# Kernel tuning notes

Hardware: AMD Instinct MI355X
Metric: run time of the kernel (lower is better)

## Reference

```python
import jax, jax.numpy as jnp
import numpy as np

B, C_IN, C_TMP, C_OUT, N = 4, 256, 256, 256, 4096


def setup_inputs() -> dict:
    key = jax.random.key(0)
    k1, k2, k3, k4 = jax.random.split(key, 4)
    scale = 1.0 / np.sqrt(C_IN)
    return {
        "fea": jax.random.normal(k1, (B, C_IN, N), dtype=jnp.float32),
        "Wq": jax.random.normal(k2, (C_TMP, C_IN), dtype=jnp.float32) * scale,
        "Wk": jax.random.normal(k3, (C_TMP, C_IN), dtype=jnp.float32) * scale,
        "Wv": jax.random.normal(k4, (C_OUT, C_IN), dtype=jnp.float32) * scale,
    }


def reference(fea, Wq, Wk, Wv):
    # 1x1 Conv1d == per-point channel matmul
    Q = jnp.einsum("ti,bin->btn", Wq, fea)   # (B, temp, N)
    K = jnp.einsum("ti,bin->btn", Wk, fea)   # (B, temp, N)
    V = jnp.einsum("oi,bin->bon", Wv, fea)   # (B, out, N)
    # S[b, i, j] = sum_t K[b, t, i] * Q[b, t, j]; note: no 1/sqrt(d) scaling
    S = jnp.einsum("bti,btj->bij", K, Q)     # (B, N, N)
    S = jax.nn.softmax(S, axis=1)            # softmax over key axis (dim=1)
    new_fea = jnp.einsum("bok,bkn->bon", V, S)  # (B, out, N)
    # merge == 'concat'
    out = jnp.concatenate([new_fea, fea], axis=1)  # (B, out+in, N)
    return jax.nn.relu(out)
```

## Files before the change

### kernel.cpp

```cpp
#include <hip/hip_runtime.h>

#define NB 4
#define C  256
#define NN 4096

typedef _Float16 half8   __attribute__((ext_vector_type(8)));
typedef _Float16 h2      __attribute__((ext_vector_type(2)));
typedef float    f32x4   __attribute__((ext_vector_type(4)));
typedef float    f32x16  __attribute__((ext_vector_type(16)));

static __device__ __forceinline__ f32x4 mfma16(half8 a, half8 b, f32x4 c) {
    return __builtin_amdgcn_mfma_f32_16x16x32_f16(a, b, c, 0, 0, 0);
}
static __device__ __forceinline__ f32x16 mfma32(half8 a, half8 b, f32x16 c) {
    return __builtin_amdgcn_mfma_f32_32x32x16_f16(a, b, c, 0, 0, 0);
}
static __device__ __forceinline__ void gld16(const void* g, void* l) {
    __builtin_amdgcn_global_load_lds(
        (const __attribute__((address_space(1))) unsigned int*)g,
        (__attribute__((address_space(3))) unsigned int*)l, 16, 0, 0);
}
static __device__ __forceinline__ h2 cvtpk(float a, float b) {
    auto r = __builtin_amdgcn_cvt_pkrtz(a, b);
    return *reinterpret_cast<h2*>(&r);
}
static __device__ __forceinline__ unsigned cvtpk_u(float a, float b) {
    auto r = __builtin_amdgcn_cvt_pkrtz(a, b);
    return *reinterpret_cast<unsigned*>(&r);
}

__global__ __launch_bounds__(256) void proj_kernel(
    const float* __restrict__ fea, const float* __restrict__ Wq,
    const float* __restrict__ Wk, const float* __restrict__ Wv,
    _Float16* __restrict__ Qt, _Float16* __restrict__ Kt,
    _Float16* __restrict__ Vp, float* __restrict__ out)
{
    const int lin = blockIdx.x + gridDim.x * blockIdx.y;
    const int xcd = lin & 7;
    const int b   = xcd >> 1;
    const int nt  = ((lin >> 3) << 1) | (xcd & 1);
    const int n0  = nt * 32;

    __shared__ __align__(16) _Float16 fh[32][264];

    const int tid = threadIdx.x;
    {
        const int nl = tid & 31, rr = tid >> 5;
        const float* feab = fea + (size_t)b * C * NN + n0 + nl;
        float* outb = out + (size_t)b * 2 * C * NN + (size_t)C * NN + n0 + nl;
#pragma unroll
        for (int p = 0; p < 32; ++p) {
            const int i = p * 8 + rr;
            const float v = feab[(size_t)i * NN];
            outb[(size_t)i * NN] = fmaxf(v, 0.f);
            fh[nl][i] = (_Float16)v;
        }
    }
    __syncthreads();

    const int w = tid >> 6, lane = tid & 63, lr = lane & 15, lg = lane >> 4;

    const float* const Ws[2] = {Wq, Wk};
    _Float16* const   Od[2] = {Qt + (size_t)b * NN * C, Kt + (size_t)b * NN * C};
#pragma unroll 1
    for (int qk = 0; qk < 2; ++qk) {
        const float* __restrict__ W = Ws[qk];
        f32x4 acc[2][4];
#pragma unroll
        for (int mi = 0; mi < 2; ++mi)
#pragma unroll
            for (int ni = 0; ni < 4; ++ni) acc[mi][ni] = (f32x4){0.f, 0.f, 0.f, 0.f};

#pragma unroll 1
        for (int kt = 0; kt < 8; ++kt) {
            half8 ah[2];
#pragma unroll
            for (int mi = 0; mi < 2; ++mi)
                ah[mi] = *(const half8*)&fh[mi * 16 + lr][kt * 32 + lg * 8];
            half8 bh[4];
#pragma unroll
            for (int ni = 0; ni < 4; ++ni) {
                const float* src = W + (size_t)(w * 64 + ni * 16 + lr) * C + kt * 32 + lg * 8;
                const float4 x0 = *(const float4*)src;
                const float4 x1 = *(const float4*)(src + 4);
                bh[ni][0] = (_Float16)x0.x; bh[ni][1] = (_Float16)x0.y;
                bh[ni][2] = (_Float16)x0.z; bh[ni][3] = (_Float16)x0.w;
                bh[ni][4] = (_Float16)x1.x; bh[ni][5] = (_Float16)x1.y;
                bh[ni][6] = (_Float16)x1.z; bh[ni][7] = (_Float16)x1.w;
            }
#pragma unroll
            for (int mi = 0; mi < 2; ++mi)
#pragma unroll
                for (int ni = 0; ni < 4; ++ni)
                    acc[mi][ni] = mfma16(ah[mi], bh[ni], acc[mi][ni]);
        }
        _Float16* dst = Od[qk];
#pragma unroll
        for (int mi = 0; mi < 2; ++mi)
#pragma unroll
            for (int ni = 0; ni < 4; ++ni)
#pragma unroll
                for (int r = 0; r < 4; ++r)
                    dst[(size_t)(n0 + mi * 16 + lg * 4 + r) * C + (w * 64 + ni * 16 + lr)] =
                        (_Float16)acc[mi][ni][r];
    }

    {
        f32x4 acc[4][2];
#pragma unroll
        for (int mi = 0; mi < 4; ++mi)
#pragma unroll
            for (int ni = 0; ni < 2; ++ni) acc[mi][ni] = (f32x4){0.f, 0.f, 0.f, 0.f};

#pragma unroll 1
        for (int kt = 0; kt < 8; ++kt) {
            half8 ah[4];
#pragma unroll
            for (int mi = 0; mi < 4; ++mi) {
                const float* src = Wv + (size_t)(w * 64 + mi * 16 + lr) * C + kt * 32 + lg * 8;
                const float4 x0 = *(const float4*)src;
                const float4 x1 = *(const float4*)(src + 4);
                ah[mi][0] = (_Float16)x0.x; ah[mi][1] = (_Float16)x0.y;
                ah[mi][2] = (_Float16)x0.z; ah[mi][3] = (_Float16)x0.w;
                ah[mi][4] = (_Float16)x1.x; ah[mi][5] = (_Float16)x1.y;
                ah[mi][6] = (_Float16)x1.z; ah[mi][7] = (_Float16)x1.w;
            }
            half8 bh[2];
#pragma unroll
            for (int ni = 0; ni < 2; ++ni)
                bh[ni] = *(const half8*)&fh[ni * 16 + lr][kt * 32 + lg * 8];
#pragma unroll
            for (int mi = 0; mi < 4; ++mi)
#pragma unroll
                for (int ni = 0; ni < 2; ++ni)
                    acc[mi][ni] = mfma16(ah[mi], bh[ni], acc[mi][ni]);
        }
        _Float16* vb = Vp + (size_t)b * C * NN;
#pragma unroll
        for (int mi = 0; mi < 4; ++mi)
#pragma unroll
            for (int ni = 0; ni < 2; ++ni)
#pragma unroll
                for (int r = 0; r < 4; ++r)
                    vb[(size_t)(w * 64 + mi * 16 + lg * 4 + r) * NN + n0 + ni * 16 + lr] =
                        (_Float16)acc[mi][ni][r];
    }
}

template<int KS>
__global__ __launch_bounds__(256, 2) void attn3(
    const _Float16* __restrict__ Qt, const _Float16* __restrict__ Kt,
    const _Float16* __restrict__ Vp, _Float16* __restrict__ Opart,
    float* __restrict__ ml, float* __restrict__ out)
{
    extern __shared__ char smem[];

    const int lin = blockIdx.x;
    const int xcd = lin & 7, slot = lin >> 3;
    int b, ks, jt;
    if constexpr (KS == 4) {
        const int combo = xcd * 2 + (slot >> 5);
        b = combo >> 2; ks = combo & 3; jt = slot & 31;
    } else {
        b = xcd >> 1; ks = 0; jt = ((slot & 15) << 1) | (xcd & 1);
    }

    const int tid = threadIdx.x;
    const int wv = tid >> 6, lane = tid & 63;
    const int l31 = lane & 31, hi = lane >> 5;
    const int j0 = jt * 128 + wv * 32;
    const int iBase = ks * (NN / KS);
    const int T = (NN / KS) / 32;

    const _Float16* Qb = Qt + (size_t)b * NN * C;
    const char* Kg = (const char*)(Kt + (size_t)b * NN * C);
    const char* Vg = (const char*)(Vp + (size_t)b * C * NN);

    half8 q[16];
#pragma unroll
    for (int kk = 0; kk < 16; ++kk)
        q[kk] = *(const half8*)(Qb + (size_t)(j0 + l31) * C + kk * 16 + hi * 8);

    h2 Om[8][8];
#pragma unroll
    for (int ob = 0; ob < 8; ++ob)
#pragma unroll
        for (int w = 0; w < 8; ++w) Om[ob][w] = (h2){0, 0};
    float m = -1e30f, ll = 0.f;

#define STAGE(nb, t_) do {                                                     \
    const int i0_ = iBase + (t_) * 32;                                         \
    char* dK_ = smem + ((nb) ? 16384 : 0);                                     \
    char* dV_ = smem + 32768 + ((nb) ? 16384 : 0);                             \
    _Pragma("unroll")                                                          \
    for (int r_ = 0; r_ < 4; ++r_) {                                           \
        const int p_ = r_ * 4096 + tid * 16;                                   \
        const int row_ = p_ >> 9, c1_ = (p_ >> 4) & 31;                        \
        gld16(Kg + (size_t)(i0_ + row_) * 512 + ((c1_ ^ row_) << 4), dK_ + p_);\
    }                                                                          \
    _Pragma("unroll")                                                          \
    for (int r_ = 0; r_ < 4; ++r_) {                                           \
        const int p_ = r_ * 4096 + tid * 16;                                   \
        const int mac_ = p_ >> 9, c1_ = (p_ >> 4) & 31;                        \
        const int o_ = mac_ * 8 + (c1_ >> 2);                                  \
        gld16(Vg + (size_t)o_ * (NN * 2) + (size_t)i0_ * 2 +                   \
                  (((c1_ & 3) ^ (mac_ & 3)) << 4), dV_ + p_);                  \
    }                                                                          \
} while (0)

    STAGE(0, 0);

#pragma unroll 1
    for (int t = 0; t < T; ++t) {
        __syncthreads();
        if (t + 1 < T) STAGE((t + 1) & 1, t + 1);

        const char* kb = smem + ((t & 1) ? 16384 : 0);
        const char* vb = smem + 32768 + ((t & 1) ? 16384 : 0);

        f32x16 s = (f32x16)(0.f);
#pragma unroll
        for (int kk = 0; kk < 16; ++kk) {
            const half8 a = *(const half8*)(kb + l31 * 512 + (((kk * 2 + hi) ^ l31) << 4));
            s = mfma32(a, q[kk], s);
        }

        float tmax = s[0];
#pragma unroll
        for (int r = 1; r < 16; ++r) tmax = fmaxf(tmax, s[r]);
        tmax = fmaxf(tmax, __shfl_xor(tmax, 32, 64));
        const float mn = fmaxf(m, tmax);
        const float sc = __expf(m - mn);
        m = mn;
        const h2 sc2 = {(_Float16)sc, (_Float16)sc};
#pragma unroll
        for (int ob = 0; ob < 8; ++ob)
#pragma unroll
            for (int w = 0; w < 8; ++w) Om[ob][w] *= sc2;

        float p[16];
        float lsum = 0.f;
#pragma unroll
        for (int r = 0; r < 16; ++r) { p[r] = __expf(s[r] - m); lsum += p[r]; }
        ll = ll * sc + lsum;

        unsigned P0 = cvtpk_u(p[0], p[1]),  P1 = cvtpk_u(p[2], p[3]);
        unsigned P2 = cvtpk_u(p[4], p[5]),  P3 = cvtpk_u(p[6], p[7]);
        unsigned P4 = cvtpk_u(p[8], p[9]),  P5 = cvtpk_u(p[10], p[11]);
        unsigned P6 = cvtpk_u(p[12], p[13]), P7 = cvtpk_u(p[14], p[15]);
        const unsigned x0 = __shfl_xor((int)P0, 32, 64), x1 = __shfl_xor((int)P1, 32, 64);
        const unsigned x2 = __shfl_xor((int)P2, 32, 64), x3 = __shfl_xor((int)P3, 32, 64);
        const unsigned x4 = __shfl_xor((int)P4, 32, 64), x5 = __shfl_xor((int)P5, 32, 64);
        const unsigned x6 = __shfl_xor((int)P6, 32, 64), x7 = __shfl_xor((int)P7, 32, 64);
        int4 fw0, fw1;
        fw0.x = hi ? x2 : P0;  fw0.y = hi ? x3 : P1;
        fw0.z = hi ? P2 : x0;  fw0.w = hi ? P3 : x1;
        fw1.x = hi ? x6 : P4;  fw1.y = hi ? x7 : P5;
        fw1.z = hi ? P6 : x4;  fw1.w = hi ? P7 : x5;
        const half8 f0 = *reinterpret_cast<half8*>(&fw0);
        const half8 f1 = *reinterpret_cast<half8*>(&fw1);

#pragma unroll
        for (int ob = 0; ob < 8; ++ob) {
            const int o = ob * 32 + l31;
            const int mac = o >> 3;
            const char* vrow = vb + mac * 512;
            const int cb = (l31 & 7) * 4;
            const int xr = l31 >> 3;
            const half8 v0 = *(const half8*)(vrow + ((cb + ((0 + hi) ^ xr)) << 4));
            const half8 v1 = *(const half8*)(vrow + ((cb + ((2 + hi) ^ xr)) << 4));
            f32x16 pacc = (f32x16)(0.f);
            pacc = mfma32(v0, f0, pacc);
            pacc = mfma32(v1, f1, pacc);
#pragma unroll
            for (int w = 0; w < 8; ++w)
                Om[ob][w] += cvtpk(pacc[2 * w], pacc[2 * w + 1]);
        }
    }

    const float lt = ll + __shfl_xor(ll, 32, 64);
    const float il = 1.f / lt;

    if constexpr (KS == 4) {
        if (hi == 0) {
            float* mlb = ml + (size_t)(b * KS + ks) * 2 * NN;
            mlb[j0 + l31] = m;
            mlb[NN + j0 + l31] = lt;
        }
        _Float16* op = Opart + (size_t)(b * KS + ks) * C * NN;
#pragma unroll
        for (int ob = 0; ob < 8; ++ob)
#pragma unroll
            for (int w = 0; w < 8; ++w) {
                const int o = ob * 32 + ((2 * w) & 3) + 8 * (w >> 1) + 4 * hi;
                op[(size_t)o * NN + j0 + l31]       = (_Float16)((float)Om[ob][w][0] * il);
                op[(size_t)(o + 1) * NN + j0 + l31] = (_Float16)((float)Om[ob][w][1] * il);
            }
    } else {
        float* obp = out + (size_t)b * 2 * C * NN;
#pragma unroll
        for (int ob = 0; ob < 8; ++ob)
#pragma unroll
            for (int w = 0; w < 8; ++w) {
                const int o = ob * 32 + ((2 * w) & 3) + 8 * (w >> 1) + 4 * hi;
                obp[(size_t)o * NN + j0 + l31]       = fmaxf((float)Om[ob][w][0] * il, 0.f);
                obp[(size_t)(o + 1) * NN + j0 + l31] = fmaxf((float)Om[ob][w][1] * il, 0.f);
            }
    }
#undef STAGE
}

template<int KS>
__global__ __launch_bounds__(256) void combine_kernel(
    const _Float16* __restrict__ Opart, const float* __restrict__ ml,
    float* __restrict__ out)
{
    const int b = blockIdx.x >> 6, cc = blockIdx.x & 63;
    const int tid = threadIdx.x;
    const int col = cc * 64 + (tid & 63);
    const int op0 = tid >> 6;
    float mv[KS], wgt[KS];
    float M = -1e30f;
#pragma unroll
    for (int s = 0; s < KS; ++s) {
        mv[s] = ml[(size_t)(b * KS + s) * 2 * NN + col];
        M = fmaxf(M, mv[s]);
    }
    float L = 0.f;
#pragma unroll
    for (int s = 0; s < KS; ++s) {
        const float lv = ml[((size_t)(b * KS + s) * 2 + 1) * NN + col];
        wgt[s] = __expf(mv[s] - M) * lv; L += wgt[s];
    }
    const float invL = 1.f / L;
#pragma unroll
    for (int s = 0; s < KS; ++s) wgt[s] *= invL;
    float* ob = out + (size_t)b * 2 * C * NN + col;
    for (int oit = 0; oit < 64; ++oit) {
        const int o = oit * 4 + op0;
        float acc = 0.f;
#pragma unroll
        for (int s = 0; s < KS; ++s)
            acc += wgt[s] * (float)Opart[((size_t)(b * KS + s) * C + o) * NN + col];
        ob[(size_t)o * NN] = fmaxf(acc, 0.f);
    }
}

extern "C" void kernel_launch(void* const* d_in, const int* in_sizes, int n_in,
                              void* d_out, int out_size, void* d_ws, size_t ws_size,
                              hipStream_t stream) {
    const float* fea = (const float*)d_in[0];
    const float* Wq  = (const float*)d_in[1];
    const float* Wk  = (const float*)d_in[2];
    const float* Wv  = (const float*)d_in[3];
    float* out = (float*)d_out;

    _Float16* Qt = (_Float16*)d_ws;
    _Float16* Kt = Qt + (size_t)NB * NN * C;
    _Float16* Vp = Kt + (size_t)NB * NN * C;
    char* extra = (char*)(Vp + (size_t)NB * NN * C);
    const size_t base = (size_t)3 * NB * NN * C * sizeof(_Float16);

    proj_kernel<<<dim3(128, 4), 256, 0, stream>>>(fea, Wq, Wk, Wv, Qt, Kt, Vp, out);

    const int SMEM = 65536;
    const size_t need4 = base + (size_t)4 * NB * C * NN * 2 + (size_t)4 * NB * 2 * NN * 4;

    if (ws_size >= need4) {
        _Float16* Op = (_Float16*)extra;
        float* mlp = (float*)(extra + (size_t)4 * NB * C * NN * 2);
        (void)hipFuncSetAttribute(reinterpret_cast<const void*>(&attn3<4>),
                                  hipFuncAttributeMaxDynamicSharedMemorySize, SMEM);
        attn3<4><<<512, 256, SMEM, stream>>>(Qt, Kt, Vp, Op, mlp, out);
        combine_kernel<4><<<NB * 64, 256, 0, stream>>>(Op, mlp, out);
    } else {
        (void)hipFuncSetAttribute(reinterpret_cast<const void*>(&attn3<1>),
                                  hipFuncAttributeMaxDynamicSharedMemorySize, SMEM);
        attn3<1><<<128, 256, SMEM, stream>>>(Qt, Kt, Vp, nullptr, nullptr, out);
    }
}
```

Measured before the change: 159.1 us.

## Accumulate attention output in fp32 MFMA registers and skip rescale lazily

The output accumulator moves from packed fp16 pairs, which needed a separate MFMA result, a convert and an add per tile, to fp32 f32x16 registers that the PV MFMAs accumulate into directly. Rescaling of the running max now happens only when some lane's tile max exceeds the current max by more than 8, which removes most per-tile scale multiplies. This doubles the accumulator register footprint (128 fp32 VGPRs) and may raise register pressure against the 2-blocks-per-CU launch bound. The lazy threshold also lets exponentials grow up to e^8 before rescaling, so fp16 P values may lose precision or saturate.

```diff
diff --git a/kernel.cpp b/kernel.cpp
--- a/kernel.cpp
+++ b/kernel.cpp
@@ -19,10 +19,6 @@
     __builtin_amdgcn_global_load_lds(
         (const __attribute__((address_space(1))) unsigned int*)g,
         (__attribute__((address_space(3))) unsigned int*)l, 16, 0, 0);
-}
-static __device__ __forceinline__ h2 cvtpk(float a, float b) {
-    auto r = __builtin_amdgcn_cvt_pkrtz(a, b);
-    return *reinterpret_cast<h2*>(&r);
 }
 static __device__ __forceinline__ unsigned cvtpk_u(float a, float b) {
     auto r = __builtin_amdgcn_cvt_pkrtz(a, b);
@@ -148,7 +144,7 @@
 }
 
 template<int KS>
-__global__ __launch_bounds__(256, 2) void attn3(
+__global__ __launch_bounds__(256, 2) void attn4(
     const _Float16* __restrict__ Qt, const _Float16* __restrict__ Kt,
     const _Float16* __restrict__ Vp, _Float16* __restrict__ Opart,
     float* __restrict__ ml, float* __restrict__ out)
@@ -181,11 +177,9 @@
     for (int kk = 0; kk < 16; ++kk)
         q[kk] = *(const half8*)(Qb + (size_t)(j0 + l31) * C + kk * 16 + hi * 8);
 
-    h2 Om[8][8];
-#pragma unroll
-    for (int ob = 0; ob < 8; ++ob)
-#pragma unroll
-        for (int w = 0; w < 8; ++w) Om[ob][w] = (h2){0, 0};
+    f32x16 O[8];
+#pragma unroll
+    for (int ob = 0; ob < 8; ++ob) O[ob] = (f32x16)(0.f);
     float m = -1e30f, ll = 0.f;
 
 #define STAGE(nb, t_) do {                                                     \
@@ -229,25 +223,24 @@
 #pragma unroll
         for (int r = 1; r < 16; ++r) tmax = fmaxf(tmax, s[r]);
         tmax = fmaxf(tmax, __shfl_xor(tmax, 32, 64));
-        const float mn = fmaxf(m, tmax);
-        const float sc = __expf(m - mn);
-        m = mn;
-        const h2 sc2 = {(_Float16)sc, (_Float16)sc};
-#pragma unroll
-        for (int ob = 0; ob < 8; ++ob)
-#pragma unroll
-            for (int w = 0; w < 8; ++w) Om[ob][w] *= sc2;
-
-        float p[16];
+        if (__any(tmax > m + 8.0f)) {
+            const float mn = fmaxf(m, tmax);
+            const float sc = __expf(m - mn);
+            m = mn;
+            ll *= sc;
+#pragma unroll
+            for (int ob = 0; ob < 8; ++ob) O[ob] *= sc;
+        }
+
         float lsum = 0.f;
 #pragma unroll
-        for (int r = 0; r < 16; ++r) { p[r] = __expf(s[r] - m); lsum += p[r]; }
-        ll = ll * sc + lsum;
-
-        unsigned P0 = cvtpk_u(p[0], p[1]),  P1 = cvtpk_u(p[2], p[3]);
-        unsigned P2 = cvtpk_u(p[4], p[5]),  P3 = cvtpk_u(p[6], p[7]);
-        unsigned P4 = cvtpk_u(p[8], p[9]),  P5 = cvtpk_u(p[10], p[11]);
-        unsigned P6 = cvtpk_u(p[12], p[13]), P7 = cvtpk_u(p[14], p[15]);
+        for (int r = 0; r < 16; ++r) { s[r] = __expf(s[r] - m); lsum += s[r]; }
+        ll += lsum;
+
+        unsigned P0 = cvtpk_u(s[0], s[1]),   P1 = cvtpk_u(s[2], s[3]);
+        unsigned P2 = cvtpk_u(s[4], s[5]),   P3 = cvtpk_u(s[6], s[7]);
+        unsigned P4 = cvtpk_u(s[8], s[9]),   P5 = cvtpk_u(s[10], s[11]);
+        unsigned P6 = cvtpk_u(s[12], s[13]), P7 = cvtpk_u(s[14], s[15]);
         const unsigned x0 = __shfl_xor((int)P0, 32, 64), x1 = __shfl_xor((int)P1, 32, 64);
         const unsigned x2 = __shfl_xor((int)P2, 32, 64), x3 = __shfl_xor((int)P3, 32, 64);
         const unsigned x4 = __shfl_xor((int)P4, 32, 64), x5 = __shfl_xor((int)P5, 32, 64);
@@ -269,12 +262,8 @@
             const int xr = l31 >> 3;
             const half8 v0 = *(const half8*)(vrow + ((cb + ((0 + hi) ^ xr)) << 4));
             const half8 v1 = *(const half8*)(vrow + ((cb + ((2 + hi) ^ xr)) << 4));
-            f32x16 pacc = (f32x16)(0.f);
-            pacc = mfma32(v0, f0, pacc);
-            pacc = mfma32(v1, f1, pacc);
-#pragma unroll
-            for (int w = 0; w < 8; ++w)
-                Om[ob][w] += cvtpk(pacc[2 * w], pacc[2 * w + 1]);
+            O[ob] = mfma32(v0, f0, O[ob]);
+            O[ob] = mfma32(v1, f1, O[ob]);
         }
     }
 
@@ -293,8 +282,8 @@
 #pragma unroll
             for (int w = 0; w < 8; ++w) {
                 const int o = ob * 32 + ((2 * w) & 3) + 8 * (w >> 1) + 4 * hi;
-                op[(size_t)o * NN + j0 + l31]       = (_Float16)((float)Om[ob][w][0] * il);
-                op[(size_t)(o + 1) * NN + j0 + l31] = (_Float16)((float)Om[ob][w][1] * il);
+                op[(size_t)o * NN + j0 + l31]       = (_Float16)(O[ob][2 * w] * il);
+                op[(size_t)(o + 1) * NN + j0 + l31] = (_Float16)(O[ob][2 * w + 1] * il);
             }
     } else {
         float* obp = out + (size_t)b * 2 * C * NN;
@@ -303,8 +292,8 @@
 #pragma unroll
             for (int w = 0; w < 8; ++w) {
                 const int o = ob * 32 + ((2 * w) & 3) + 8 * (w >> 1) + 4 * hi;
-                obp[(size_t)o * NN + j0 + l31]       = fmaxf((float)Om[ob][w][0] * il, 0.f);
-                obp[(size_t)(o + 1) * NN + j0 + l31] = fmaxf((float)Om[ob][w][1] * il, 0.f);
+                obp[(size_t)o * NN + j0 + l31]       = fmaxf(O[ob][2 * w] * il, 0.f);
+                obp[(size_t)(o + 1) * NN + j0 + l31] = fmaxf(O[ob][2 * w + 1] * il, 0.f);
             }
     }
 #undef STAGE
@@ -369,13 +358,13 @@
     if (ws_size >= need4) {
         _Float16* Op = (_Float16*)extra;
         float* mlp = (float*)(extra + (size_t)4 * NB * C * NN * 2);
-        (void)hipFuncSetAttribute(reinterpret_cast<const void*>(&attn3<4>),
+        (void)hipFuncSetAttribute(reinterpret_cast<const void*>(&attn4<4>),
                                   hipFuncAttributeMaxDynamicSharedMemorySize, SMEM);
-        attn3<4><<<512, 256, SMEM, stream>>>(Qt, Kt, Vp, Op, mlp, out);
+        attn4<4><<<512, 256, SMEM, stream>>>(Qt, Kt, Vp, Op, mlp, out);
         combine_kernel<4><<<NB * 64, 256, 0, stream>>>(Op, mlp, out);
     } else {
-        (void)hipFuncSetAttribute(reinterpret_cast<const void*>(&attn3<1>),
+        (void)hipFuncSetAttribute(reinterpret_cast<const void*>(&attn4<1>),
                                   hipFuncAttributeMaxDynamicSharedMemorySize, SMEM);
-        attn3<1><<<128, 256, SMEM, stream>>>(Qt, Kt, Vp, nullptr, nullptr, out);
-    }
-}
+        attn4<1><<<128, 256, SMEM, stream>>>(Qt, Kt, Vp, nullptr, nullptr, out);
+    }
+}
```

Result: no change. 158.2 us (-0.5%).
